# Performance work log

Hardware: AMD Instinct MI355X
Metric: run time of the kernel (lower is better)

The kernel has to match this reference:

```python
import jax, jax.numpy as jnp
import numpy as np

N, E, D_FEAT, D_HID, N_CLASS, N_LAYER = 100000, 1600000, 128, 128, 40, 2


def _sage_layer(x, x_, src, dst, wl, wr, b, n):
    # mean aggregation of neighbor (src) features into dst nodes
    agg = jax.ops.segment_sum(x[src], dst, num_segments=n)          # [N, d_in]
    cnt = jax.ops.segment_sum(jnp.ones((src.shape[0], 1), x.dtype), dst, num_segments=n)
    agg = agg / jnp.maximum(cnt, 1.0)
    h = agg @ wl + x @ wr + b        # neighbor path + root path
    h_ = x_ @ wr + b                 # twin (detached-root) stream: root weight only
    return jax.nn.relu(h), jax.nn.relu(h_)


def setup_inputs() -> dict:
    key = jax.random.key(0)
    ks = jax.random.split(key, 12)
    s = 1.0 / np.sqrt(D_HID)
    inp = {
        "x": jax.random.normal(ks[0], (N, D_FEAT), jnp.float32),
        "edge_index1": jax.random.randint(ks[1], (2, E), 0, N, jnp.int32),
        "edge_index2": jax.random.randint(ks[2], (2, E), 0, N, jnp.int32),
        "wl1": jax.random.uniform(ks[3], (D_FEAT, D_HID), jnp.float32, -s, s),
        "wr1": jax.random.uniform(ks[4], (D_FEAT, D_HID), jnp.float32, -s, s),
        "b1": jnp.zeros((D_HID,), jnp.float32),
        "wl2": jax.random.uniform(ks[5], (D_HID, D_HID), jnp.float32, -s, s),
        "wr2": jax.random.uniform(ks[6], (D_HID, D_HID), jnp.float32, -s, s),
        "b2": jnp.zeros((D_HID,), jnp.float32),
        "w_out": jax.random.uniform(ks[7], (D_HID * N_LAYER, N_CLASS), jnp.float32, -s, s),
        "b_out": jnp.zeros((N_CLASS,), jnp.float32),
        "batch_size": N,
    }
    return inp


def reference(x, edge_index1, edge_index2, wl1, wr1, b1, wl2, wr2, b2, w_out, b_out, batch_size):
    n = x.shape[0]
    x_ = jax.lax.stop_gradient(x)[:batch_size]   # detached twin stream of root nodes
    # layer 1 (dropout is eval-mode no-op)
    h1, h1_ = _sage_layer(x, x_, edge_index1[0], edge_index1[1], wl1, wr1, b1, n)
    # layer 2
    h2, h2_ = _sage_layer(h1, h1_, edge_index2[0], edge_index2[1], wl2, wr2, b2, n)
    # jumping knowledge: mode 'cat' over per-layer root representations
    h = jnp.concatenate([h1[:batch_size], h2[:batch_size]], axis=-1)
    return h @ w_out + b_out
```

## Files before the change

kernel.cpp:

```cpp
#include <hip/hip_runtime.h>


#define MAXB  512
#define CAP   24
#define CAPS  6144
#define PBLK  384

typedef __attribute__((ext_vector_type(8))) short short8;
typedef __attribute__((ext_vector_type(4))) float floatx4;

__device__ __forceinline__ unsigned short f2b(float f) {
    unsigned u = __float_as_uint(f);
    unsigned r = (u + 0x7fffu + ((u >> 16) & 1u)) >> 16;
    return (unsigned short)r;
}
__device__ __forceinline__ float lo2f(unsigned u) { return __uint_as_float(u << 16); }
__device__ __forceinline__ float hi2f(unsigned u) { return __uint_as_float(u & 0xffff0000u); }
__device__ __forceinline__ unsigned pack2(float a, float b) {
    return (unsigned)f2b(a) | ((unsigned)f2b(b) << 16);
}

__global__ __launch_bounds__(256)
void prep_all(const float4* __restrict__ x4, uint4* __restrict__ xb4, long n8,
              const float* __restrict__ wl1, const float* __restrict__ wr1,
              const float* __restrict__ wl2, const float* __restrict__ wr2,
              const float* __restrict__ wo,
              unsigned short* __restrict__ wt1, unsigned short* __restrict__ wt2,
              unsigned short* __restrict__ wot, int* __restrict__ zero_region) {
    long i = (long)blockIdx.x * 256 + threadIdx.x;
    if (i < 2048) zero_region[i] = 0;
    if (i < n8) {
        float4 a = x4[i * 2];
        float4 b = x4[i * 2 + 1];
        uint4 o;
        o.x = pack2(a.x, a.y); o.y = pack2(a.z, a.w);
        o.z = pack2(b.x, b.y); o.w = pack2(b.z, b.w);
        xb4[i] = o;
    }
    if (i < 65536) {
        int l = (int)(i >> 15);
        int k5 = (int)(i & 32767);
        int j = k5 & 7, lane = (k5 >> 3) & 63, kb = (k5 >> 9) & 7, c = k5 >> 12;
        int k = kb * 32 + (lane >> 4) * 8 + j;
        int n = c * 16 + (lane & 15);
        const float* Wl = l ? wl2 : wl1;
        const float* Wr = l ? wr2 : wr1;
        float v = (k < 128) ? Wl[k * 128 + n] : Wr[(k - 128) * 128 + n];
        (l ? wt2 : wt1)[k5] = f2b(v);
    } else if (i < 65536 + 12288) {
        int k5 = (int)(i - 65536);
        int j = k5 & 7, lane = (k5 >> 3) & 63, kb = (k5 >> 9) & 7, c = k5 >> 12;
        int k = kb * 32 + (lane >> 4) * 8 + j;
        int col = c * 16 + (lane & 15);
        float v = (col < 40) ? wo[k * 40 + col] : 0.0f;
        wot[k5] = f2b(v);
    }
}

__global__ __launch_bounds__(256)
void bucket_hist2(const int* __restrict__ dst1, const int* __restrict__ dst2,
                  int* __restrict__ hist1, int* __restrict__ hist2, int E, int nb) {
    __shared__ int h[MAXB];
    const int* dst = blockIdx.y ? dst2 : dst1;
    int* hist      = blockIdx.y ? hist2 : hist1;
    for (int i = threadIdx.x; i < nb; i += 256) h[i] = 0;
    __syncthreads();
    for (int e = blockIdx.x * 256 + threadIdx.x; e < E; e += gridDim.x * 256)
        atomicAdd(&h[dst[e] >> 8], 1);
    __syncthreads();
    for (int i = threadIdx.x; i < nb; i += 256)
        if (h[i]) atomicAdd(&hist[i], h[i]);
}

__global__ __launch_bounds__(256)
void bucket_scan2(const int* __restrict__ hist1, const int* __restrict__ hist2,
                  int* __restrict__ bptr1, int* __restrict__ bptr2, int nb, int E) {
    __shared__ int pair[256];
    const int* hist = blockIdx.x ? hist2 : hist1;
    int* bptr       = blockIdx.x ? bptr2 : bptr1;
    int t = threadIdx.x;
    int v0 = (2 * t < nb) ? hist[2 * t] : 0;
    int v1 = (2 * t + 1 < nb) ? hist[2 * t + 1] : 0;
    pair[t] = v0 + v1;
    __syncthreads();
    for (int off = 1; off < 256; off <<= 1) {
        int y = (t >= off) ? pair[t - off] : 0;
        __syncthreads();
        pair[t] += y;
        __syncthreads();
    }
    int ebase = pair[t] - (v0 + v1);
    if (2 * t < nb)     bptr[2 * t]     = ebase;
    if (2 * t + 1 < nb) bptr[2 * t + 1] = ebase + v0;
    if (t == 0) bptr[nb] = E;
}

__global__ __launch_bounds__(256)
void partition_edges2(const int* __restrict__ ei1, const int* __restrict__ ei2,
                      const int* __restrict__ bptr1, const int* __restrict__ bptr2,
                      int* __restrict__ gcur1, int* __restrict__ gcur2,
                      int* __restrict__ part1, int* __restrict__ part2,
                      int E, int nb) {
    __shared__ unsigned stage[MAXB][CAP];
    __shared__ int lcnt[MAXB];
    const int* src  = blockIdx.y ? ei2 : ei1;
    const int* dst  = src + E;
    const int* bptr = blockIdx.y ? bptr2 : bptr1;
    int* gcur       = blockIdx.y ? gcur2 : gcur1;
    int* part       = blockIdx.y ? part2 : part1;
    const int t = threadIdx.x;
    for (int i = t; i < nb; i += 256) lcnt[i] = 0;
    __syncthreads();
    const int per = (E + gridDim.x - 1) / gridDim.x;
    const int e0 = blockIdx.x * per;
    const int e1 = min(e0 + per, E);
    for (int e = e0 + t; e < e1; e += 256) {
        int d = dst[e];
        int b = d >> 8;
        unsigned rec = (unsigned)src[e] | ((unsigned)(d & 255) << 17);
        int p = atomicAdd(&lcnt[b], 1);
        if (p < CAP) stage[b][p] = rec;
        else {
            int g = atomicAdd(&gcur[b], 1);
            part[bptr[b] + g] = (int)rec;
        }
    }
    __syncthreads();
    for (int b = t; b < nb; b += 256) {
        int c = lcnt[b]; if (c > CAP) c = CAP;
        if (c > 0) {
            int g = atomicAdd(&gcur[b], c);
            int base = bptr[b] + g;
            for (int i = 0; i < c; ++i) part[base + i] = (int)stage[b][i];
        }
    }
}

__global__ __launch_bounds__(256)
void node_sort2(const int* __restrict__ bptr1, const int* __restrict__ bptr2,
                const int* __restrict__ part1, const int* __restrict__ part2,
                int* __restrict__ col1, int* __restrict__ col2,
                int* __restrict__ row_ptr1, int* __restrict__ row_ptr2,
                int N, int E) {
    __shared__ int recs[CAPS];
    __shared__ int sorted[CAPS];
    __shared__ int hcnt[256];
    __shared__ int hoff[256];
    const int* bptr = blockIdx.y ? bptr2 : bptr1;
    const int* part = blockIdx.y ? part2 : part1;
    int* col        = blockIdx.y ? col2 : col1;
    int* row_ptr    = blockIdx.y ? row_ptr2 : row_ptr1;
    const int b = blockIdx.x, t = threadIdx.x;
    const int beg = bptr[b], end = bptr[b + 1];
    int cnt = end - beg;
    if (cnt > CAPS) cnt = CAPS;

    for (int i = t; i < cnt; i += 256) recs[i] = part[beg + i];
    hcnt[t] = 0;
    __syncthreads();
    for (int i = t; i < cnt; i += 256)
        atomicAdd(&hcnt[((unsigned)recs[i]) >> 17], 1);
    __syncthreads();

    int v = hcnt[t];
    hoff[t] = v;
    __syncthreads();
    for (int off = 1; off < 256; off <<= 1) {
        int y = (t >= off) ? hoff[t - off] : 0;
        __syncthreads();
        hoff[t] += y;
        __syncthreads();
    }
    int myoff = hoff[t] - v;

    int row = b * 256 + t;
    if (row <= N) row_ptr[row] = beg + myoff;
    if (b == gridDim.x - 1 && t == 0) row_ptr[N] = E;
    __syncthreads();
    hoff[t] = myoff;
    hcnt[t] = 0;
    __syncthreads();

    for (int i = t; i < cnt; i += 256) {
        unsigned rec = (unsigned)recs[i];
        int node = rec >> 17;
        int p = hoff[node] + atomicAdd(&hcnt[node], 1);
        sorted[p] = (int)(rec & 0x1FFFF);
    }
    __syncthreads();
    for (int i = t; i < cnt; i += 256) col[beg + i] = sorted[i];
}

__global__ __launch_bounds__(256)
void gather_mean_b16(const uint4* __restrict__ xb, const int* __restrict__ row_ptr,
                     const int* __restrict__ col, uint4* __restrict__ agg, int N) {
    int gid  = blockIdx.x * 256 + threadIdx.x;
    int node = gid >> 4;
    int lane = gid & 15;
    if (node >= N) return;
    int beg = row_ptr[node], end = row_ptr[node + 1];
    float acc[8];
#pragma unroll
    for (int j = 0; j < 8; ++j) acc[j] = 0.0f;
    int e = beg;
    if (e + 8 <= end) {
        int cidx[8];
#pragma unroll
        for (int q = 0; q < 8; ++q) cidx[q] = col[e + q];
        for (;;) {
            uint4 v[8];
#pragma unroll
            for (int q = 0; q < 8; ++q) v[q] = xb[(size_t)cidx[q] * 16 + lane];
            e += 8;
            const bool more = (e + 8 <= end);
            if (more) {
#pragma unroll
                for (int q = 0; q < 8; ++q) cidx[q] = col[e + q];
            }
#pragma unroll
            for (int q = 0; q < 8; ++q) {
                acc[0] += lo2f(v[q].x); acc[1] += hi2f(v[q].x);
                acc[2] += lo2f(v[q].y); acc[3] += hi2f(v[q].y);
                acc[4] += lo2f(v[q].z); acc[5] += hi2f(v[q].z);
                acc[6] += lo2f(v[q].w); acc[7] += hi2f(v[q].w);
            }
            if (!more) break;
        }
    }
    for (; e + 3 < end; e += 4) {
        uint4 v[4];
#pragma unroll
        for (int q = 0; q < 4; ++q) v[q] = xb[(size_t)col[e + q] * 16 + lane];
#pragma unroll
        for (int q = 0; q < 4; ++q) {
            acc[0] += lo2f(v[q].x); acc[1] += hi2f(v[q].x);
            acc[2] += lo2f(v[q].y); acc[3] += hi2f(v[q].y);
            acc[4] += lo2f(v[q].z); acc[5] += hi2f(v[q].z);
            acc[6] += lo2f(v[q].w); acc[7] += hi2f(v[q].w);
        }
    }
    for (; e < end; ++e) {
        uint4 v0 = xb[(size_t)col[e] * 16 + lane];
        acc[0] += lo2f(v0.x); acc[1] += hi2f(v0.x);
        acc[2] += lo2f(v0.y); acc[3] += hi2f(v0.y);
        acc[4] += lo2f(v0.z); acc[5] += hi2f(v0.z);
        acc[6] += lo2f(v0.w); acc[7] += hi2f(v0.w);
    }
    float inv = 1.0f / fmaxf((float)(end - beg), 1.0f);
#pragma unroll
    for (int j = 0; j < 8; ++j) acc[j] *= inv;
    uint4 o;
    o.x = pack2(acc[0], acc[1]); o.y = pack2(acc[2], acc[3]);
    o.z = pack2(acc[4], acc[5]); o.w = pack2(acc[6], acc[7]);
    agg[(size_t)node * 16 + lane] = o;
}

__global__ __launch_bounds__(256)
void sage_gemm_mfma(const unsigned short* __restrict__ Aggb,
                    const unsigned short* __restrict__ Xb,
                    const unsigned short* __restrict__ Wt,
                    const float* __restrict__ bias,
                    unsigned short* __restrict__ Hb, int N) {
    const int wave = threadIdx.x >> 6;
    const int lane = threadIdx.x & 63;
    const int quad = lane >> 4;
    const int l16  = lane & 15;
    const int rowbase = blockIdx.x * 128 + wave * 32;

    floatx4 acc[2][8];
#pragma unroll
    for (int r = 0; r < 2; ++r)
#pragma unroll
        for (int c = 0; c < 8; ++c) acc[r][c] = (floatx4){0.f, 0.f, 0.f, 0.f};

    int arow0 = rowbase + l16;      if (arow0 >= N) arow0 = N - 1;
    int arow1 = rowbase + 16 + l16; if (arow1 >= N) arow1 = N - 1;
    const size_t aoff0 = (size_t)arow0 * 128 + quad * 8;
    const size_t aoff1 = (size_t)arow1 * 128 + quad * 8;

#pragma unroll
    for (int kb = 0; kb < 8; ++kb) {
        const unsigned short* Ab = (kb < 4) ? Aggb : Xb;
        const int koff = (kb & 3) * 32;
        short8 a0 = __builtin_bit_cast(short8, *(const uint4*)(Ab + aoff0 + koff));
        short8 a1 = __builtin_bit_cast(short8, *(const uint4*)(Ab + aoff1 + koff));
#pragma unroll
        for (int c = 0; c < 8; ++c) {
            short8 b = __builtin_bit_cast(short8,
                *(const uint4*)(Wt + (size_t)(((c * 8 + kb) * 64 + lane) * 8)));
            acc[0][c] = __builtin_amdgcn_mfma_f32_16x16x32_bf16(a0, b, acc[0][c], 0, 0, 0);
            acc[1][c] = __builtin_amdgcn_mfma_f32_16x16x32_bf16(a1, b, acc[1][c], 0, 0, 0);
        }
    }

    float bcol[8];
#pragma unroll
    for (int c = 0; c < 8; ++c) bcol[c] = bias[c * 16 + l16];
#pragma unroll
    for (int r = 0; r < 2; ++r)
#pragma unroll
        for (int i = 0; i < 4; ++i) {
            int row = rowbase + r * 16 + quad * 4 + i;
            if (row < N) {
#pragma unroll
                for (int c = 0; c < 8; ++c)
                    Hb[(size_t)row * 128 + c * 16 + l16] =
                        f2b(fmaxf(acc[r][c][i] + bcol[c], 0.f));
            }
        }
}

__global__ __launch_bounds__(256)
void out_gemm_mfma(const unsigned short* __restrict__ H1b,
                   const unsigned short* __restrict__ H2b,
                   const unsigned short* __restrict__ Wot,
                   const float* __restrict__ bo,
                   float* __restrict__ out, int N) {
    const int wave = threadIdx.x >> 6;
    const int lane = threadIdx.x & 63;
    const int quad = lane >> 4;
    const int l16  = lane & 15;
    const int rowbase = blockIdx.x * 128 + wave * 32;

    floatx4 acc[2][3];
#pragma unroll
    for (int r = 0; r < 2; ++r)
#pragma unroll
        for (int c = 0; c < 3; ++c) acc[r][c] = (floatx4){0.f, 0.f, 0.f, 0.f};

    int arow0 = rowbase + l16;      if (arow0 >= N) arow0 = N - 1;
    int arow1 = rowbase + 16 + l16; if (arow1 >= N) arow1 = N - 1;
    const size_t aoff0 = (size_t)arow0 * 128 + quad * 8;
    const size_t aoff1 = (size_t)arow1 * 128 + quad * 8;

#pragma unroll
    for (int kb = 0; kb < 8; ++kb) {
        const unsigned short* Ab = (kb < 4) ? H1b : H2b;
        const int koff = (kb & 3) * 32;
        short8 a0 = __builtin_bit_cast(short8, *(const uint4*)(Ab + aoff0 + koff));
        short8 a1 = __builtin_bit_cast(short8, *(const uint4*)(Ab + aoff1 + koff));
#pragma unroll
        for (int c = 0; c < 3; ++c) {
            short8 b = __builtin_bit_cast(short8,
                *(const uint4*)(Wot + (size_t)(((c * 8 + kb) * 64 + lane) * 8)));
            acc[0][c] = __builtin_amdgcn_mfma_f32_16x16x32_bf16(a0, b, acc[0][c], 0, 0, 0);
            acc[1][c] = __builtin_amdgcn_mfma_f32_16x16x32_bf16(a1, b, acc[1][c], 0, 0, 0);
        }
    }

    float bcol[3];
#pragma unroll
    for (int c = 0; c < 3; ++c) {
        int colc = c * 16 + l16;
        bcol[c] = (colc < 40) ? bo[colc] : 0.f;
    }
#pragma unroll
    for (int r = 0; r < 2; ++r)
#pragma unroll
        for (int i = 0; i < 4; ++i) {
            int row = rowbase + r * 16 + quad * 4 + i;
            if (row < N) {
#pragma unroll
                for (int c = 0; c < 3; ++c) {
                    int colc = c * 16 + l16;
                    if (colc < 40)
                        out[(size_t)row * 40 + colc] = acc[r][c][i] + bcol[c];
                }
            }
        }
}

extern "C" void kernel_launch(void* const* d_in, const int* in_sizes, int n_in,
                              void* d_out, int out_size, void* d_ws, size_t ws_size,
                              hipStream_t stream) {
    const float* x     = (const float*)d_in[0];
    const int*   ei1   = (const int*)d_in[1];
    const int*   ei2   = (const int*)d_in[2];
    const float* wl1   = (const float*)d_in[3];
    const float* wr1   = (const float*)d_in[4];
    const float* b1    = (const float*)d_in[5];
    const float* wl2   = (const float*)d_in[6];
    const float* wr2   = (const float*)d_in[7];
    const float* b2    = (const float*)d_in[8];
    const float* w_out = (const float*)d_in[9];
    const float* b_out = (const float*)d_in[10];

    const int N  = in_sizes[0] / 128;
    const int E  = in_sizes[1] / 2;
    const int nb = (N + 255) >> 8;

    int* hist1    = (int*)d_ws;
    int* gcur1    = hist1 + 512;
    int* hist2    = gcur1 + 512;
    int* gcur2    = hist2 + 512;
    int* bptr1    = gcur2 + 512;
    int* bptr2    = bptr1 + 513;
    int* row_ptr1 = bptr2 + 513;
    int* row_ptr2 = row_ptr1 + (N + 1);
    int* part1    = row_ptr2 + (N + 1);
    int* col1     = part1 + E;
    int* part2    = col1 + E;
    int* col2     = part2 + E;
    size_t int_cnt = (size_t)(2048 + 1026 + 2 * (N + 1)) + (size_t)4 * E;
    int_cnt = (int_cnt + 3) & ~(size_t)3;
    unsigned short* xb   = (unsigned short*)((int*)d_ws + int_cnt);
    unsigned short* h1b  = xb  + (size_t)N * 128;
    unsigned short* h2b  = h1b + (size_t)N * 128;
    unsigned short* aggb = h2b + (size_t)N * 128;
    unsigned short* wt1  = aggb + (size_t)N * 128;
    unsigned short* wt2  = wt1 + 32768;
    unsigned short* wot  = wt2 + 32768;

    const long n8         = (long)N * 128 / 8;
    const int prep_blocks = (int)((n8 + 255) / 256);
    const int gath_blocks = (int)(((size_t)N * 16 + 255) / 256);
    const int mfma_blocks = (N + 127) / 128;

    prep_all<<<prep_blocks, 256, 0, stream>>>(
        (const float4*)x, (uint4*)xb, n8, wl1, wr1, wl2, wr2, w_out,
        wt1, wt2, wot, hist1);

    bucket_hist2<<<dim3(256, 2), 256, 0, stream>>>(ei1 + E, ei2 + E, hist1, hist2, E, nb);
    bucket_scan2<<<2, 256, 0, stream>>>(hist1, hist2, bptr1, bptr2, nb, E);
    partition_edges2<<<dim3(PBLK, 2), 256, 0, stream>>>(
        ei1, ei2, bptr1, bptr2, gcur1, gcur2, part1, part2, E, nb);
    node_sort2<<<dim3(nb, 2), 256, 0, stream>>>(
        bptr1, bptr2, part1, part2, col1, col2, row_ptr1, row_ptr2, N, E);

    gather_mean_b16<<<gath_blocks, 256, 0, stream>>>((const uint4*)xb, row_ptr1,
                                                     col1, (uint4*)aggb, N);
    sage_gemm_mfma<<<mfma_blocks, 256, 0, stream>>>(aggb, xb, wt1, b1, h1b, N);
    gather_mean_b16<<<gath_blocks, 256, 0, stream>>>((const uint4*)h1b, row_ptr2,
                                                     col2, (uint4*)aggb, N);
    sage_gemm_mfma<<<mfma_blocks, 256, 0, stream>>>(aggb, h1b, wt2, b2, h2b, N);

    out_gemm_mfma<<<mfma_blocks, 256, 0, stream>>>(h1b, h2b, wot, b_out,
                                                   (float*)d_out, N);
}
```

Baseline: 445.5 us.

## Fuse neighbor gather with MFMA GEMM per 16-node tile and fold output projection

```diff
diff --git a/kernel.cpp b/kernel.cpp
--- a/kernel.cpp
+++ b/kernel.cpp
@@ -21,14 +21,15 @@
 }
 
 __global__ __launch_bounds__(256)
-void prep_all(const float4* __restrict__ x4, uint4* __restrict__ xb4, long n8,
-              const float* __restrict__ wl1, const float* __restrict__ wr1,
-              const float* __restrict__ wl2, const float* __restrict__ wr2,
-              const float* __restrict__ wo,
-              unsigned short* __restrict__ wt1, unsigned short* __restrict__ wt2,
-              unsigned short* __restrict__ wot, int* __restrict__ zero_region) {
+void prep_hist(const float4* __restrict__ x4, uint4* __restrict__ xb4, long n8,
+               const float* __restrict__ wl1, const float* __restrict__ wr1,
+               const float* __restrict__ wl2, const float* __restrict__ wr2,
+               const float* __restrict__ wo,
+               unsigned short* __restrict__ wt1, unsigned short* __restrict__ wt2,
+               unsigned short* __restrict__ wot,
+               const int* __restrict__ dst1, const int* __restrict__ dst2,
+               int* __restrict__ hist1, int* __restrict__ hist2, int E, int nb) {
     long i = (long)blockIdx.x * 256 + threadIdx.x;
-    if (i < 2048) zero_region[i] = 0;
     if (i < n8) {
         float4 a = x4[i * 2];
         float4 b = x4[i * 2 + 1];
@@ -55,21 +56,20 @@
         float v = (col < 40) ? wo[k * 40 + col] : 0.0f;
         wot[k5] = f2b(v);
     }
-}
-
-__global__ __launch_bounds__(256)
-void bucket_hist2(const int* __restrict__ dst1, const int* __restrict__ dst2,
-                  int* __restrict__ hist1, int* __restrict__ hist2, int E, int nb) {
     __shared__ int h[MAXB];
-    const int* dst = blockIdx.y ? dst2 : dst1;
-    int* hist      = blockIdx.y ? hist2 : hist1;
-    for (int i = threadIdx.x; i < nb; i += 256) h[i] = 0;
-    __syncthreads();
-    for (int e = blockIdx.x * 256 + threadIdx.x; e < E; e += gridDim.x * 256)
-        atomicAdd(&h[dst[e] >> 8], 1);
-    __syncthreads();
-    for (int i = threadIdx.x; i < nb; i += 256)
-        if (h[i]) atomicAdd(&hist[i], h[i]);
+    if (blockIdx.x < 512) {
+        const int layer = blockIdx.x >> 8;
+        const int bx    = blockIdx.x & 255;
+        const int* dst  = layer ? dst2 : dst1;
+        int* hist       = layer ? hist2 : hist1;
+        for (int k = threadIdx.x; k < nb; k += 256) h[k] = 0;
+        __syncthreads();
+        for (int e = bx * 256 + threadIdx.x; e < E; e += 256 * 256)
+            atomicAdd(&h[dst[e] >> 8], 1);
+        __syncthreads();
+        for (int k = threadIdx.x; k < nb; k += 256)
+            if (h[k]) atomicAdd(&hist[k], h[k]);
+    }
 }
 
 __global__ __launch_bounds__(256)
@@ -191,17 +191,10 @@
     for (int i = t; i < cnt; i += 256) col[beg + i] = sorted[i];
 }
 
-__global__ __launch_bounds__(256)
-void gather_mean_b16(const uint4* __restrict__ xb, const int* __restrict__ row_ptr,
-                     const int* __restrict__ col, uint4* __restrict__ agg, int N) {
-    int gid  = blockIdx.x * 256 + threadIdx.x;
-    int node = gid >> 4;
-    int lane = gid & 15;
-    if (node >= N) return;
-    int beg = row_ptr[node], end = row_ptr[node + 1];
-    float acc[8];
-#pragma unroll
-    for (int j = 0; j < 8; ++j) acc[j] = 0.0f;
+__device__ __forceinline__ void gather_node(const uint4* __restrict__ xb,
+                                            const int* __restrict__ col,
+                                            int beg, int end, int lane,
+                                            float acc[8]) {
     int e = beg;
     if (e + 8 <= end) {
         int cidx[8];
@@ -249,125 +242,170 @@
     float inv = 1.0f / fmaxf((float)(end - beg), 1.0f);
 #pragma unroll
     for (int j = 0; j < 8; ++j) acc[j] *= inv;
-    uint4 o;
-    o.x = pack2(acc[0], acc[1]); o.y = pack2(acc[2], acc[3]);
-    o.z = pack2(acc[4], acc[5]); o.w = pack2(acc[6], acc[7]);
-    agg[(size_t)node * 16 + lane] = o;
-}
-
-__global__ __launch_bounds__(256)
-void sage_gemm_mfma(const unsigned short* __restrict__ Aggb,
-                    const unsigned short* __restrict__ Xb,
-                    const unsigned short* __restrict__ Wt,
-                    const float* __restrict__ bias,
-                    unsigned short* __restrict__ Hb, int N) {
-    const int wave = threadIdx.x >> 6;
-    const int lane = threadIdx.x & 63;
+}
+
+#define LDS_SLOT(row, col4) ((row) * 16 + ((col4) ^ ((row) & 7)))
+
+__global__ __launch_bounds__(256)
+void fused_layer1(const uint4* __restrict__ xb, const int* __restrict__ row_ptr,
+                  const int* __restrict__ col,
+                  const unsigned short* __restrict__ Wt,
+                  const float* __restrict__ bias,
+                  unsigned short* __restrict__ Hb, int N) {
+    __shared__ uint4 lds[16 * 16];
+    const int t = threadIdx.x;
+    {
+        const int lrow = t >> 4;
+        const int lane = t & 15;
+        const int node = blockIdx.x * 16 + lrow;
+        float acc[8];
+#pragma unroll
+        for (int j = 0; j < 8; ++j) acc[j] = 0.0f;
+        if (node < N)
+            gather_node(xb, col, row_ptr[node], row_ptr[node + 1], lane, acc);
+        uint4 o;
+        o.x = pack2(acc[0], acc[1]); o.y = pack2(acc[2], acc[3]);
+        o.z = pack2(acc[4], acc[5]); o.w = pack2(acc[6], acc[7]);
+        lds[LDS_SLOT(lrow, lane)] = o;
+    }
+    __syncthreads();
+
+    const int wave = t >> 6;
+    const int lane = t & 63;
     const int quad = lane >> 4;
     const int l16  = lane & 15;
-    const int rowbase = blockIdx.x * 128 + wave * 32;
-
-    floatx4 acc[2][8];
-#pragma unroll
-    for (int r = 0; r < 2; ++r)
-#pragma unroll
-        for (int c = 0; c < 8; ++c) acc[r][c] = (floatx4){0.f, 0.f, 0.f, 0.f};
-
-    int arow0 = rowbase + l16;      if (arow0 >= N) arow0 = N - 1;
-    int arow1 = rowbase + 16 + l16; if (arow1 >= N) arow1 = N - 1;
-    const size_t aoff0 = (size_t)arow0 * 128 + quad * 8;
-    const size_t aoff1 = (size_t)arow1 * 128 + quad * 8;
+    const int rowbase = blockIdx.x * 16;
+
+    floatx4 acc2[2] = {(floatx4){0.f,0.f,0.f,0.f}, (floatx4){0.f,0.f,0.f,0.f}};
+    int arow = rowbase + l16; if (arow >= N) arow = N - 1;
+    const unsigned short* Xs = (const unsigned short*)xb;
+    const size_t aoff = (size_t)arow * 128 + quad * 8;
 
 #pragma unroll
     for (int kb = 0; kb < 8; ++kb) {
-        const unsigned short* Ab = (kb < 4) ? Aggb : Xb;
-        const int koff = (kb & 3) * 32;
-        short8 a0 = __builtin_bit_cast(short8, *(const uint4*)(Ab + aoff0 + koff));
-        short8 a1 = __builtin_bit_cast(short8, *(const uint4*)(Ab + aoff1 + koff));
-#pragma unroll
-        for (int c = 0; c < 8; ++c) {
+        short8 a;
+        if (kb < 4)
+            a = __builtin_bit_cast(short8, lds[LDS_SLOT(l16, quad + (kb & 3) * 4)]);
+        else
+            a = __builtin_bit_cast(short8, *(const uint4*)(Xs + aoff + (kb & 3) * 32));
+#pragma unroll
+        for (int cc = 0; cc < 2; ++cc) {
+            const int c = wave * 2 + cc;
             short8 b = __builtin_bit_cast(short8,
                 *(const uint4*)(Wt + (size_t)(((c * 8 + kb) * 64 + lane) * 8)));
-            acc[0][c] = __builtin_amdgcn_mfma_f32_16x16x32_bf16(a0, b, acc[0][c], 0, 0, 0);
-            acc[1][c] = __builtin_amdgcn_mfma_f32_16x16x32_bf16(a1, b, acc[1][c], 0, 0, 0);
-        }
-    }
-
-    float bcol[8];
-#pragma unroll
-    for (int c = 0; c < 8; ++c) bcol[c] = bias[c * 16 + l16];
-#pragma unroll
-    for (int r = 0; r < 2; ++r)
+            acc2[cc] = __builtin_amdgcn_mfma_f32_16x16x32_bf16(a, b, acc2[cc], 0, 0, 0);
+        }
+    }
+
+#pragma unroll
+    for (int cc = 0; cc < 2; ++cc) {
+        const int c = wave * 2 + cc;
+        const float bc = bias[c * 16 + l16];
 #pragma unroll
         for (int i = 0; i < 4; ++i) {
-            int row = rowbase + r * 16 + quad * 4 + i;
-            if (row < N) {
-#pragma unroll
-                for (int c = 0; c < 8; ++c)
-                    Hb[(size_t)row * 128 + c * 16 + l16] =
-                        f2b(fmaxf(acc[r][c][i] + bcol[c], 0.f));
-            }
-        }
-}
-
-__global__ __launch_bounds__(256)
-void out_gemm_mfma(const unsigned short* __restrict__ H1b,
-                   const unsigned short* __restrict__ H2b,
-                   const unsigned short* __restrict__ Wot,
-                   const float* __restrict__ bo,
-                   float* __restrict__ out, int N) {
-    const int wave = threadIdx.x >> 6;
-    const int lane = threadIdx.x & 63;
+            int row = rowbase + quad * 4 + i;
+            if (row < N)
+                Hb[(size_t)row * 128 + c * 16 + l16] = f2b(fmaxf(acc2[cc][i] + bc, 0.f));
+        }
+    }
+}
+
+__global__ __launch_bounds__(256)
+void fused_layer2(const uint4* __restrict__ h1b4, const int* __restrict__ row_ptr,
+                  const int* __restrict__ col,
+                  const unsigned short* __restrict__ Wt,
+                  const float* __restrict__ bias,
+                  const unsigned short* __restrict__ Wot,
+                  const float* __restrict__ bo,
+                  float* __restrict__ out, int N) {
+    __shared__ uint4 lds[16 * 16];
+    const int t = threadIdx.x;
+    {
+        const int lrow = t >> 4;
+        const int lane = t & 15;
+        const int node = blockIdx.x * 16 + lrow;
+        float acc[8];
+#pragma unroll
+        for (int j = 0; j < 8; ++j) acc[j] = 0.0f;
+        if (node < N)
+            gather_node(h1b4, col, row_ptr[node], row_ptr[node + 1], lane, acc);
+        uint4 o;
+        o.x = pack2(acc[0], acc[1]); o.y = pack2(acc[2], acc[3]);
+        o.z = pack2(acc[4], acc[5]); o.w = pack2(acc[6], acc[7]);
+        lds[LDS_SLOT(lrow, lane)] = o;
+    }
+    __syncthreads();
+
+    const int wave = t >> 6;
+    const int lane = t & 63;
     const int quad = lane >> 4;
     const int l16  = lane & 15;
-    const int rowbase = blockIdx.x * 128 + wave * 32;
-
-    floatx4 acc[2][3];
-#pragma unroll
-    for (int r = 0; r < 2; ++r)
-#pragma unroll
-        for (int c = 0; c < 3; ++c) acc[r][c] = (floatx4){0.f, 0.f, 0.f, 0.f};
-
-    int arow0 = rowbase + l16;      if (arow0 >= N) arow0 = N - 1;
-    int arow1 = rowbase + 16 + l16; if (arow1 >= N) arow1 = N - 1;
-    const size_t aoff0 = (size_t)arow0 * 128 + quad * 8;
-    const size_t aoff1 = (size_t)arow1 * 128 + quad * 8;
+    const int rowbase = blockIdx.x * 16;
+
+    floatx4 acc2[2] = {(floatx4){0.f,0.f,0.f,0.f}, (floatx4){0.f,0.f,0.f,0.f}};
+    floatx4 accO    = (floatx4){0.f,0.f,0.f,0.f};
+    int arow = rowbase + l16; if (arow >= N) arow = N - 1;
+    const unsigned short* H1s = (const unsigned short*)h1b4;
+    const size_t aoff = (size_t)arow * 128 + quad * 8;
 
 #pragma unroll
     for (int kb = 0; kb < 8; ++kb) {
-        const unsigned short* Ab = (kb < 4) ? H1b : H2b;
-        const int koff = (kb & 3) * 32;
-        short8 a0 = __builtin_bit_cast(short8, *(const uint4*)(Ab + aoff0 + koff));
-        short8 a1 = __builtin_bit_cast(short8, *(const uint4*)(Ab + aoff1 + koff));
-#pragma unroll
-        for (int c = 0; c < 3; ++c) {
+        short8 a;
+        if (kb < 4)
+            a = __builtin_bit_cast(short8, lds[LDS_SLOT(l16, quad + (kb & 3) * 4)]);
+        else
+            a = __builtin_bit_cast(short8, *(const uint4*)(H1s + aoff + (kb & 3) * 32));
+#pragma unroll
+        for (int cc = 0; cc < 2; ++cc) {
+            const int c = wave * 2 + cc;
             short8 b = __builtin_bit_cast(short8,
-                *(const uint4*)(Wot + (size_t)(((c * 8 + kb) * 64 + lane) * 8)));
-            acc[0][c] = __builtin_amdgcn_mfma_f32_16x16x32_bf16(a0, b, acc[0][c], 0, 0, 0);
-            acc[1][c] = __builtin_amdgcn_mfma_f32_16x16x32_bf16(a1, b, acc[1][c], 0, 0, 0);
-        }
-    }
-
-    float bcol[3];
-#pragma unroll
-    for (int c = 0; c < 3; ++c) {
-        int colc = c * 16 + l16;
-        bcol[c] = (colc < 40) ? bo[colc] : 0.f;
-    }
-#pragma unroll
-    for (int r = 0; r < 2; ++r)
-#pragma unroll
-        for (int i = 0; i < 4; ++i) {
-            int row = rowbase + r * 16 + quad * 4 + i;
-            if (row < N) {
-#pragma unroll
-                for (int c = 0; c < 3; ++c) {
-                    int colc = c * 16 + l16;
-                    if (colc < 40)
-                        out[(size_t)row * 40 + colc] = acc[r][c][i] + bcol[c];
-                }
+                *(const uint4*)(Wt + (size_t)(((c * 8 + kb) * 64 + lane) * 8)));
+            acc2[cc] = __builtin_amdgcn_mfma_f32_16x16x32_bf16(a, b, acc2[cc], 0, 0, 0);
+        }
+        if (kb >= 4 && wave < 3) {
+            short8 b = __builtin_bit_cast(short8,
+                *(const uint4*)(Wot + (size_t)(((wave * 8 + (kb - 4)) * 64 + lane) * 8)));
+            accO = __builtin_amdgcn_mfma_f32_16x16x32_bf16(a, b, accO, 0, 0, 0);
+        }
+    }
+
+    __syncthreads();
+    {
+        unsigned short* lds16 = (unsigned short*)lds;
+#pragma unroll
+        for (int cc = 0; cc < 2; ++cc) {
+            const int c = wave * 2 + cc;
+            const float bc = bias[c * 16 + l16];
+            const int colc = c * 16 + l16;
+            const int col4 = colc >> 3;
+#pragma unroll
+            for (int i = 0; i < 4; ++i) {
+                const int lrow = quad * 4 + i;
+                lds16[LDS_SLOT(lrow, col4) * 8 + (colc & 7)] =
+                    f2b(fmaxf(acc2[cc][i] + bc, 0.f));
             }
         }
+    }
+    __syncthreads();
+
+    if (wave < 3) {
+#pragma unroll
+        for (int kh = 0; kh < 4; ++kh) {
+            short8 a = __builtin_bit_cast(short8, lds[LDS_SLOT(l16, quad + kh * 4)]);
+            short8 b = __builtin_bit_cast(short8,
+                *(const uint4*)(Wot + (size_t)(((wave * 8 + 4 + kh) * 64 + lane) * 8)));
+            accO = __builtin_amdgcn_mfma_f32_16x16x32_bf16(a, b, accO, 0, 0, 0);
+        }
+        const int colc = wave * 16 + l16;
+        if (colc < 40) {
+            const float bco = bo[colc];
+#pragma unroll
+            for (int i = 0; i < 4; ++i) {
+                int row = rowbase + quad * 4 + i;
+                if (row < N) out[(size_t)row * 40 + colc] = accO[i] + bco;
+            }
+        }
+    }
 }
 
 extern "C" void kernel_launch(void* const* d_in, const int* in_sizes, int n_in,
@@ -405,35 +443,29 @@
     int_cnt = (int_cnt + 3) & ~(size_t)3;
     unsigned short* xb   = (unsigned short*)((int*)d_ws + int_cnt);
     unsigned short* h1b  = xb  + (size_t)N * 128;
-    unsigned short* h2b  = h1b + (size_t)N * 128;
-    unsigned short* aggb = h2b + (size_t)N * 128;
-    unsigned short* wt1  = aggb + (size_t)N * 128;
+    unsigned short* wt1  = h1b + (size_t)N * 128;
     unsigned short* wt2  = wt1 + 32768;
     unsigned short* wot  = wt2 + 32768;
 
     const long n8         = (long)N * 128 / 8;
     const int prep_blocks = (int)((n8 + 255) / 256);
-    const int gath_blocks = (int)(((size_t)N * 16 + 255) / 256);
-    const int mfma_blocks = (N + 127) / 128;
-
-    prep_all<<<prep_blocks, 256, 0, stream>>>(
+    const int tile_blocks = (N + 15) / 16;
+
+    hipMemsetAsync(hist1, 0, 2048 * sizeof(int), stream);
+
+    prep_hist<<<prep_blocks, 256, 0, stream>>>(
         (const float4*)x, (uint4*)xb, n8, wl1, wr1, wl2, wr2, w_out,
-        wt1, wt2, wot, hist1);
-
-    bucket_hist2<<<dim3(256, 2), 256, 0, stream>>>(ei1 + E, ei2 + E, hist1, hist2, E, nb);
+        wt1, wt2, wot, ei1 + E, ei2 + E, hist1, hist2, E, nb);
+
     bucket_scan2<<<2, 256, 0, stream>>>(hist1, hist2, bptr1, bptr2, nb, E);
     partition_edges2<<<dim3(PBLK, 2), 256, 0, stream>>>(
         ei1, ei2, bptr1, bptr2, gcur1, gcur2, part1, part2, E, nb);
     node_sort2<<<dim3(nb, 2), 256, 0, stream>>>(
         bptr1, bptr2, part1, part2, col1, col2, row_ptr1, row_ptr2, N, E);
 
-    gather_mean_b16<<<gath_blocks, 256, 0, stream>>>((const uint4*)xb, row_ptr1,
-                                                     col1, (uint4*)aggb, N);
-    sage_gemm_mfma<<<mfma_blocks, 256, 0, stream>>>(aggb, xb, wt1, b1, h1b, N);
-    gather_mean_b16<<<gath_blocks, 256, 0, stream>>>((const uint4*)h1b, row_ptr2,
-                                                     col2, (uint4*)aggb, N);
-    sage_gemm_mfma<<<mfma_blocks, 256, 0, stream>>>(aggb, h1b, wt2, b2, h2b, N);
-
-    out_gemm_mfma<<<mfma_blocks, 256, 0, stream>>>(h1b, h2b, wot, b_out,
-                                                   (float*)d_out, N);
-}
+    fused_layer1<<<tile_blocks, 256, 0, stream>>>(
+        (const uint4*)xb, row_ptr1, col1, wt1, b1, h1b, N);
+    fused_layer2<<<tile_blocks, 256, 0, stream>>>(
+        (const uint4*)h1b, row_ptr2, col2, wt2, b2, wot, b_out,
+        (float*)d_out, N);
+}
```

Result: faster. 381.7 us, median of 2 (-14.3%).
